# Kernel optimization log

Measured on AMD Instinct MI355X. Metric: run time of the kernel, lower is better.

The kernel has to match this reference:

```python
import jax, jax.numpy as jnp
import numpy as np

N, D, E, H, TOP_K = 4096, 1024, 8, 2048, 2


def setup_inputs() -> dict:
    key = jax.random.key(0)
    kx, kr, k1, kb1, k2, kb2 = jax.random.split(key, 6)
    x = jax.random.normal(kx, (N, D), dtype=jnp.float32)
    # top-2 sparse routing scores: zeros mark non-routed (token, expert) pairs
    r = jax.random.uniform(kr, (N, E), dtype=jnp.float32)
    thresh = jax.lax.top_k(r, TOP_K)[0][:, -1:]
    routing = jnp.where(r >= thresh, r, 0.0)
    # Expert params, torch Linear init scale (uniform +-1/sqrt(fan_in))
    s1 = 1.0 / np.sqrt(D)
    s2 = 1.0 / np.sqrt(H)
    W1 = jax.random.uniform(k1, (E, D, H), dtype=jnp.float32, minval=-s1, maxval=s1)
    b1 = jax.random.uniform(kb1, (E, H), dtype=jnp.float32, minval=-s1, maxval=s1)
    W2 = jax.random.uniform(k2, (E, H, D), dtype=jnp.float32, minval=-s2, maxval=s2)
    b2 = jax.random.uniform(kb2, (E, D), dtype=jnp.float32, minval=-s2, maxval=s2)
    return {"x": x, "routing": routing, "W1": W1, "b1": b1, "W2": W2, "b2": b2}


def reference(x, routing, W1, b1, W2, b2):
    # Each expert is Linear(D,H) -> GELU -> Linear(H,D); per-token output is
    # sum over experts of routing[n,e] * expert_e(x[n]). Tokens with routing==0
    # contribute exactly zero, matching the masked gather/scatter in the original.
    h = jax.nn.gelu(jnp.einsum('nd,edh->neh', x, W1) + b1[None], approximate=False)  # [N,E,H]
    y = jnp.einsum('neh,ehd->ned', h, W2) + b2[None]                                  # [N,E,D]
    return jnp.einsum('ned,ne->nd', y, routing)                                       # [N,D]
```

## Files before the change

kernel.cpp:

```cpp
#include <hip/hip_runtime.h>
#include <hip/hip_bf16.h>

#define NTOK 4096
#define DIM  1024
#define NEXP 8
#define HID  2048
#define HROWS 8448

typedef __attribute__((ext_vector_type(8))) __bf16 bf16x8;
typedef __attribute__((ext_vector_type(4))) float  f32x4;
typedef __attribute__((address_space(1))) const unsigned char gconst_u8;
typedef __attribute__((address_space(3))) unsigned char lds_u8;

__device__ __forceinline__ unsigned short f2bf(float f) {
    unsigned u = __float_as_uint(f);
    u += 0x7fffu + ((u >> 16) & 1u);
    return (unsigned short)(u >> 16);
}

__device__ __forceinline__ void gload16(const void* g, void* l) {
    __builtin_amdgcn_global_load_lds((gconst_u8*)g, (lds_u8*)l, 16, 0, 0);
}

#define WAITK(N) asm volatile("s_waitcnt vmcnt(" #N ") lgkmcnt(0)" ::: "memory")
#define BAR() do { __builtin_amdgcn_s_barrier(); __builtin_amdgcn_sched_barrier(0); } while (0)

__global__ __launch_bounds__(256) void prep(
    const float* __restrict__ x, const float* __restrict__ routing,
    const float* __restrict__ W1,
    unsigned short* __restrict__ xbf, unsigned short* __restrict__ W1F,
    int* __restrict__ counts, int* __restrict__ lists,
    int* __restrict__ slotrec, int* __restrict__ scnt)
{
    const int bid = blockIdx.x;
    const int t = threadIdx.x;
    if (bid >= 4096) {
        int n = (bid - 4096) * 256 + t;
        if (n >= NTOK) return;
        int sc = 0;
        #pragma unroll
        for (int e = 0; e < NEXP; ++e) {
            if (routing[n * NEXP + e] > 0.0f) {
                int i = atomicAdd(&counts[e], 1);
                if (i < NTOK) {
                    lists[e * NTOK + i] = n;
                    if (sc < 4) slotrec[n * 4 + sc] = (e << 20) | i;
                    ++sc;
                }
            }
        }
        scnt[n] = sc;
        return;
    }
    if (bid >= 2048) {
        int i = ((bid - 2048) * 256 + t) * 8;
        float4 a = *(const float4*)(x + i);
        float4 b = *(const float4*)(x + i + 4);
        unsigned short v[8];
        v[0] = f2bf(a.x); v[1] = f2bf(a.y); v[2] = f2bf(a.z); v[3] = f2bf(a.w);
        v[4] = f2bf(b.x); v[5] = f2bf(b.y); v[6] = f2bf(b.z); v[7] = f2bf(b.w);
        *(uint4*)(xbf + i) = *(const uint4*)v;
        return;
    }
    int e = bid >> 8, ks = (bid >> 3) & 31, fblk = bid & 7;
    const float* src = W1 + ((size_t)e * DIM + ks * 32) * HID + fblk * 256;
    unsigned short* dst = W1F + (((size_t)(e * 32 + ks) * 128) + fblk * 16) * 512;
    __shared__ unsigned short lds[32][264];
    const int kr = t >> 3, ch = t & 7;
    #pragma unroll
    for (int q = 0; q < 8; ++q) {
        float4 f4 = *(const float4*)(src + (size_t)kr * HID + ch * 32 + q * 4);
        int c = ch * 32 + q * 4;
        lds[kr][c + 0] = f2bf(f4.x); lds[kr][c + 1] = f2bf(f4.y);
        lds[kr][c + 2] = f2bf(f4.z); lds[kr][c + 3] = f2bf(f4.w);
    }
    __syncthreads();
    uint4* dv = (uint4*)dst;
    #pragma unroll
    for (int i = 0; i < 4; ++i) {
        int Q = t + 256 * i;
        int fl = Q >> 6, l = Q & 63;
        int cb = fl * 16 + (l & 15), rb = (l >> 4) * 8;
        unsigned short v[8];
        #pragma unroll
        for (int j = 0; j < 8; ++j) v[j] = lds[rb + j][cb];
        dv[Q] = *(const uint4*)v;
    }
}

__global__ __launch_bounds__(512, 4) void gemm1_gelu(
    const unsigned short* __restrict__ xbf, const unsigned short* __restrict__ W1F,
    const float* __restrict__ b1, const int* __restrict__ counts,
    const int* __restrict__ lists, unsigned short* __restrict__ h,
    const float* __restrict__ W2, unsigned short* __restrict__ W2F)
{
    __shared__ uint4 SM[4608];
    const int bid = blockIdx.x;
    const int t = threadIdx.x;

    if (bid >= 768) {
        const int unit = bid - 768;
        const int e = unit & 7, ks = (unit >> 3) & 63, half = unit >> 9;
        const float* src = W2 + ((size_t)e * HID + ks * 32) * DIM + half * 512;
        unsigned short* lds = (unsigned short*)SM;
        const int kr = t >> 4, ch = t & 15;
        #pragma unroll
        for (int q = 0; q < 8; ++q) {
            float4 f4 = *(const float4*)(src + (size_t)kr * DIM + ch * 32 + q * 4);
            int c = ch * 32 + q * 4;
            lds[kr * 520 + c + 0] = f2bf(f4.x); lds[kr * 520 + c + 1] = f2bf(f4.y);
            lds[kr * 520 + c + 2] = f2bf(f4.z); lds[kr * 520 + c + 3] = f2bf(f4.w);
        }
        __syncthreads();
        uint4* dv = (uint4*)(W2F + (((size_t)(e * 64 + ks)) * 64 + half * 32) * 512);
        #pragma unroll
        for (int i = 0; i < 4; ++i) {
            int Q = t + 512 * i;
            int fl = Q >> 6, l = Q & 63;
            int cb = fl * 16 + (l & 15), rb = (l >> 4) * 8;
            unsigned short v[8];
            #pragma unroll
            for (int j = 0; j < 8; ++j) v[j] = lds[(rb + j) * 520 + cb];
            dv[Q] = *(const uint4*)v;
        }
        return;
    }

    const int e  = bid & 7;
    const int q  = bid >> 3;
    const int mt = q % 6;
    const int nt = q / 6;

    int cnt = counts[e];
    int off = 0;
    #pragma unroll
    for (int j = 0; j < NEXP; ++j) if (j < e) off += counts[j];
    if (off + cnt > HROWS) cnt = HROWS - off;
    const int m0 = mt * 256;
    if (m0 >= cnt) return;

    const int lane = t & 63;
    const int wid  = t >> 6;
    const int wm   = wid >> 1;
    const int wn   = wid & 1;

    const int gi0 = m0 + wid * 16 + (lane & 15);
    const int gi1 = gi0 + 128;
    const int tok0 = lists[e * NTOK + ((gi0 < cnt) ? gi0 : 0)];
    const int tok1 = lists[e * NTOK + ((gi1 < cnt) ? gi1 : 0)];
    const unsigned short* ag0 = xbf + (size_t)tok0 * DIM + (lane >> 4) * 8;
    const unsigned short* ag1 = xbf + (size_t)tok1 * DIM + (lane >> 4) * 8;

    const unsigned short* bg = W1F + ((size_t)(e * 32) * 128 + nt * 8 + wid) * 512 + lane * 8;

    f32x4 acc[4][4];
    #pragma unroll
    for (int m = 0; m < 4; ++m)
        #pragma unroll
        for (int n = 0; n < 4; ++n) acc[m][n] = (f32x4){0.f, 0.f, 0.f, 0.f};

#define STG1(P, KS) do { \
        gload16(ag0 + (KS) * 32, (P) + wid * 64); \
        gload16(ag1 + (KS) * 32, (P) + (wid + 8) * 64); \
        gload16(bg + (size_t)(KS) * 65536, (P) + 1024 + wid * 64); \
    } while (0)
#define CMP1(P) do { \
        const bf16x8* Af = (const bf16x8*)(P); \
        const bf16x8* Bf = (const bf16x8*)((P) + 1024); \
        bf16x8 af[4], bfr[4]; \
        _Pragma("unroll") for (int m = 0; m < 4; ++m) af[m] = Af[((wm * 4 + m) << 6) | lane]; \
        _Pragma("unroll") for (int n = 0; n < 4; ++n) bfr[n] = Bf[((wn * 4 + n) << 6) | lane]; \
        __builtin_amdgcn_s_setprio(1); \
        _Pragma("unroll") for (int m = 0; m < 4; ++m) \
            _Pragma("unroll") for (int n = 0; n < 4; ++n) \
                acc[m][n] = __builtin_amdgcn_mfma_f32_16x16x32_bf16(af[m], bfr[n], acc[m][n], 0, 0, 0); \
        __builtin_amdgcn_s_setprio(0); \
    } while (0)

    uint4 *P0 = SM, *P1 = SM + 1536, *P2 = SM + 3072;
    STG1(P0, 0);
    STG1(P1, 1);
    for (int T = 0; T < 30; ++T) {
        WAITK(3);
        BAR();
        STG1(P2, T + 2);
        CMP1(P0);
        uint4* tmp = P0; P0 = P1; P1 = P2; P2 = tmp;
    }
    WAITK(3); BAR(); CMP1(P0);
    { uint4* tmp = P0; P0 = P1; P1 = P2; P2 = tmp; }
    WAITK(0); BAR(); CMP1(P0);
#undef STG1
#undef CMP1

    asm volatile("s_waitcnt lgkmcnt(0)" ::: "memory");
    BAR();
    unsigned short* hb = (unsigned short*)SM;
    const int lg = lane >> 4;
    #pragma unroll
    for (int n = 0; n < 4; ++n) {
        const int cl = (wn * 4 + n) * 16 + (lane & 15);
        const float bb = b1[e * HID + nt * 128 + cl];
        #pragma unroll
        for (int m = 0; m < 4; ++m) {
            const int il = (wm * 4 + m) * 16 + (lg << 2);
            const int scl = cl ^ (lg << 4);
            #pragma unroll
            for (int r = 0; r < 4; ++r) {
                float v = acc[m][n][r] + bb;
                float g = 0.5f * v * (1.0f + erff(v * 0.70710678118654752f));
                hb[(il + r) * 144 + scl] = f2bf(g);
            }
        }
    }
    __syncthreads();
    #pragma unroll
    for (int s = 0; s < 8; ++s) {
        const int row = s * 32 + (t >> 4);
        if (m0 + row < cnt) {
            const int p = t & 15;
            const int gblk = ((p >> 1) ^ ((row >> 2) & 3));
            const int gc = gblk * 16 + (p & 1) * 8;
            uint4 v = *(const uint4*)(hb + row * 144 + p * 8);
            *(uint4*)(h + (size_t)(off + m0 + row) * HID + nt * 128 + gc) = v;
        }
    }
}

__global__ __launch_bounds__(256, 4) void gemm2_store(
    const unsigned short* __restrict__ h, const unsigned short* __restrict__ W2F,
    const float* __restrict__ b2, const int* __restrict__ counts,
    const int* __restrict__ lists, const float* __restrict__ routing,
    float* __restrict__ cbuf)
{
    const int id = blockIdx.x;
    const int e  = id & 7;
    const int nt = (id >> 3) & 7;
    const int mt = id >> 6;

    int cnt = counts[e];
    int off = 0;
    #pragma unroll
    for (int j = 0; j < NEXP; ++j) if (j < e) off += counts[j];
    if (off + cnt > HROWS) cnt = HROWS - off;
    const int m0 = mt * 128;
    if (m0 >= cnt) return;

    __shared__ uint4 SM[3072];

    const int t    = threadIdx.x;
    const int lane = t & 63;
    const int wid  = t >> 6;
    const int wm   = wid >> 1;
    const int wn   = wid & 1;

    const int r0 = off + m0 + wid * 16 + (lane & 15);
    const unsigned short* ag0 = h + (size_t)r0 * HID + (lane >> 4) * 8;
    const unsigned short* ag1 = ag0 + (size_t)64 * HID;

    const unsigned short* bg0 = W2F + ((size_t)(e * 64) * 64 + nt * 8 + wid) * 512 + lane * 8;
    const unsigned short* bg1 = bg0 + 4 * 512;

    f32x4 acc[4][4];
    #pragma unroll
    for (int m = 0; m < 4; ++m)
        #pragma unroll
        for (int n = 0; n < 4; ++n) acc[m][n] = (f32x4){0.f, 0.f, 0.f, 0.f};

#define STG2(P, KS) do { \
        gload16(ag0 + (KS) * 32, (P) + wid * 64); \
        gload16(ag1 + (KS) * 32, (P) + (wid + 4) * 64); \
        gload16(bg0 + (size_t)(KS) * 32768, (P) + 512 + wid * 64); \
        gload16(bg1 + (size_t)(KS) * 32768, (P) + 512 + (wid + 4) * 64); \
    } while (0)
#define CMP2(P) do { \
        const bf16x8* Af = (const bf16x8*)(P); \
        const bf16x8* Bf = (const bf16x8*)((P) + 512); \
        bf16x8 af[4], bfr[4]; \
        _Pragma("unroll") for (int m = 0; m < 4; ++m) af[m] = Af[((wm * 4 + m) << 6) | lane]; \
        _Pragma("unroll") for (int n = 0; n < 4; ++n) bfr[n] = Bf[((wn * 4 + n) << 6) | lane]; \
        __builtin_amdgcn_s_setprio(1); \
        _Pragma("unroll") for (int m = 0; m < 4; ++m) \
            _Pragma("unroll") for (int n = 0; n < 4; ++n) \
                acc[m][n] = __builtin_amdgcn_mfma_f32_16x16x32_bf16(af[m], bfr[n], acc[m][n], 0, 0, 0); \
        __builtin_amdgcn_s_setprio(0); \
    } while (0)

    uint4 *P0 = SM, *P1 = SM + 1024, *P2 = SM + 2048;
    STG2(P0, 0);
    STG2(P1, 1);
    for (int T = 0; T < 62; ++T) {
        WAITK(4);
        BAR();
        STG2(P2, T + 2);
        CMP2(P0);
        uint4* tmp = P0; P0 = P1; P1 = P2; P2 = tmp;
    }
    WAITK(4); BAR(); CMP2(P0);
    { uint4* tmp = P0; P0 = P1; P1 = P2; P2 = tmp; }
    WAITK(0); BAR(); CMP2(P0);
#undef STG2
#undef CMP2

    const int n0 = nt * 128;
    int cols[4]; float bb[4];
    #pragma unroll
    for (int n = 0; n < 4; ++n) {
        cols[n] = n0 + (wn * 4 + n) * 16 + (lane & 15);
        bb[n] = b2[e * DIM + cols[n]];
    }
    #pragma unroll
    for (int m = 0; m < 4; ++m) {
        const int ib = m0 + (wm * 4 + m) * 16 + ((lane >> 4) << 2);
        #pragma unroll
        for (int r = 0; r < 4; ++r) {
            const int i = ib + r;
            if (i < cnt) {
                const int token = lists[e * NTOK + i];
                const float wt = routing[token * NEXP + e];
                float* dst = cbuf + (size_t)(off + i) * DIM;
                #pragma unroll
                for (int n = 0; n < 4; ++n)
                    dst[cols[n]] = wt * (acc[m][n][r] + bb[n]);
            }
        }
    }
}

__global__ __launch_bounds__(256) void combine(
    const float* __restrict__ cbuf, const int* __restrict__ counts,
    const int* __restrict__ slotrec, const int* __restrict__ scnt,
    float* __restrict__ out)
{
    const int n = blockIdx.x;
    const int t = threadIdx.x;
    int offs[NEXP];
    int s = 0;
    #pragma unroll
    for (int e = 0; e < NEXP; ++e) { offs[e] = s; s += counts[e]; }
    int sc = scnt[n]; if (sc > 4) sc = 4;
    float4 acc = {0.f, 0.f, 0.f, 0.f};
    for (int j = 0; j < sc; ++j) {
        int rec = slotrec[n * 4 + j];
        int e = rec >> 20, i = rec & 0xFFFFF;
        float4 v = ((const float4*)(cbuf + (size_t)(offs[e] + i) * DIM))[t];
        acc.x += v.x; acc.y += v.y; acc.z += v.z; acc.w += v.w;
    }
    ((float4*)(out + (size_t)n * DIM))[t] = acc;
}

extern "C" void kernel_launch(void* const* d_in, const int* in_sizes, int n_in,
                              void* d_out, int out_size, void* d_ws, size_t ws_size,
                              hipStream_t stream) {
    const float* x       = (const float*)d_in[0];
    const float* routing = (const float*)d_in[1];
    const float* W1      = (const float*)d_in[2];
    const float* b1      = (const float*)d_in[3];
    const float* W2      = (const float*)d_in[4];
    const float* b2      = (const float*)d_in[5];
    float* out = (float*)d_out;

    char* ws = (char*)d_ws;
    int* counts          = (int*)ws;
    int* lists           = (int*)(ws + 0x400);
    int* slotrec         = (int*)(ws + 0x20400);
    int* scnt            = (int*)(ws + 0x30400);
    unsigned short* xbf  = (unsigned short*)(ws + 0x40000);
    float*          cbuf = (float*)(ws + 0x40000);
    unsigned short* W1F  = (unsigned short*)(ws + 0x840000);
    unsigned short* W2F  = (unsigned short*)(ws + 0x2840000);
    unsigned short* h    = (unsigned short*)(ws + 0x4840000);

    hipMemsetAsync(counts, 0, 256, stream);
    prep<<<4112, 256, 0, stream>>>(x, routing, W1, xbf, W1F,
                                   counts, lists, slotrec, scnt);
    gemm1_gelu<<<1792, 512, 0, stream>>>(xbf, W1F, b1, counts, lists, h, W2, W2F);
    gemm2_store<<<768, 256, 0, stream>>>(h, W2F, b2, counts, lists, routing, cbuf);
    combine<<<NTOK, 256, 0, stream>>>(cbuf, counts, slotrec, scnt, out);
}
```

Before: 185.4 us.

## Load A operand directly into registers, stage only B through LDS

In both expert GEMM kernels the A operand (gathered token rows of xbf, or rows of h) is no longer staged through LDS. Each wave loads its own fragments straight into registers with vector global loads, and only the B weight tiles keep the triple-buffered global_load_lds pipeline. The A loads are issued after each compute step, and the wait counts are adjusted to match. This cuts LDS traffic and footprint, which could raise occupancy, but the A loads are now duplicated across the wn waves and have less latency hiding. The prep kernels also pad their LDS transpose rows differently to avoid bank conflicts.

New measurement: 281.3 us. +51.7%, slower.

```diff
diff --git a/kernel.cpp b/kernel.cpp
--- a/kernel.cpp
+++ b/kernel.cpp
@@ -24,6 +24,7 @@
 
 #define WAITK(N) asm volatile("s_waitcnt vmcnt(" #N ") lgkmcnt(0)" ::: "memory")
 #define BAR() do { __builtin_amdgcn_s_barrier(); __builtin_amdgcn_sched_barrier(0); } while (0)
+#define SFENCE() __builtin_amdgcn_sched_barrier(0)
 
 __global__ __launch_bounds__(256) void prep(
     const float* __restrict__ x, const float* __restrict__ routing,
@@ -65,7 +66,7 @@
     int e = bid >> 8, ks = (bid >> 3) & 31, fblk = bid & 7;
     const float* src = W1 + ((size_t)e * DIM + ks * 32) * HID + fblk * 256;
     unsigned short* dst = W1F + (((size_t)(e * 32 + ks) * 128) + fblk * 16) * 512;
-    __shared__ unsigned short lds[32][264];
+    __shared__ unsigned short lds[32][266];
     const int kr = t >> 3, ch = t & 7;
     #pragma unroll
     for (int q = 0; q < 8; ++q) {
@@ -108,8 +109,8 @@
         for (int q = 0; q < 8; ++q) {
             float4 f4 = *(const float4*)(src + (size_t)kr * DIM + ch * 32 + q * 4);
             int c = ch * 32 + q * 4;
-            lds[kr * 520 + c + 0] = f2bf(f4.x); lds[kr * 520 + c + 1] = f2bf(f4.y);
-            lds[kr * 520 + c + 2] = f2bf(f4.z); lds[kr * 520 + c + 3] = f2bf(f4.w);
+            lds[kr * 522 + c + 0] = f2bf(f4.x); lds[kr * 522 + c + 1] = f2bf(f4.y);
+            lds[kr * 522 + c + 2] = f2bf(f4.z); lds[kr * 522 + c + 3] = f2bf(f4.w);
         }
         __syncthreads();
         uint4* dv = (uint4*)(W2F + (((size_t)(e * 64 + ks)) * 64 + half * 32) * 512);
@@ -120,7 +121,7 @@
             int cb = fl * 16 + (l & 15), rb = (l >> 4) * 8;
             unsigned short v[8];
             #pragma unroll
-            for (int j = 0; j < 8; ++j) v[j] = lds[(rb + j) * 520 + cb];
+            for (int j = 0; j < 8; ++j) v[j] = lds[(rb + j) * 522 + cb];
             dv[Q] = *(const uint4*)v;
         }
         return;
@@ -143,13 +144,15 @@
     const int wid  = t >> 6;
     const int wm   = wid >> 1;
     const int wn   = wid & 1;
-
-    const int gi0 = m0 + wid * 16 + (lane & 15);
-    const int gi1 = gi0 + 128;
-    const int tok0 = lists[e * NTOK + ((gi0 < cnt) ? gi0 : 0)];
-    const int tok1 = lists[e * NTOK + ((gi1 < cnt) ? gi1 : 0)];
-    const unsigned short* ag0 = xbf + (size_t)tok0 * DIM + (lane >> 4) * 8;
-    const unsigned short* ag1 = xbf + (size_t)tok1 * DIM + (lane >> 4) * 8;
+    const int lane15 = lane & 15;
+
+    unsigned aoff[4];
+    #pragma unroll
+    for (int m = 0; m < 4; ++m) {
+        int r = m0 + (wm * 4 + m) * 16 + lane15;
+        int tok = lists[e * NTOK + ((r < cnt) ? r : 0)];
+        aoff[m] = (unsigned)tok * DIM + ((lane >> 4) << 3);
+    }
 
     const unsigned short* bg = W1F + ((size_t)(e * 32) * 128 + nt * 8 + wid) * 512 + lane * 8;
 
@@ -159,37 +162,43 @@
         #pragma unroll
         for (int n = 0; n < 4; ++n) acc[m][n] = (f32x4){0.f, 0.f, 0.f, 0.f};
 
-#define STG1(P, KS) do { \
-        gload16(ag0 + (KS) * 32, (P) + wid * 64); \
-        gload16(ag1 + (KS) * 32, (P) + (wid + 8) * 64); \
-        gload16(bg + (size_t)(KS) * 65536, (P) + 1024 + wid * 64); \
+    bf16x8 ar[4];
+
+#define LDA1(KS) do { \
+        _Pragma("unroll") for (int m = 0; m < 4; ++m) \
+            ar[m] = *(const bf16x8*)(xbf + aoff[m] + (KS) * 32); \
     } while (0)
+#define STG1(P, KS) gload16(bg + (size_t)(KS) * 65536, (P) + wid * 64)
 #define CMP1(P) do { \
-        const bf16x8* Af = (const bf16x8*)(P); \
-        const bf16x8* Bf = (const bf16x8*)((P) + 1024); \
-        bf16x8 af[4], bfr[4]; \
-        _Pragma("unroll") for (int m = 0; m < 4; ++m) af[m] = Af[((wm * 4 + m) << 6) | lane]; \
+        const bf16x8* Bf = (const bf16x8*)(P); \
+        bf16x8 bfr[4]; \
         _Pragma("unroll") for (int n = 0; n < 4; ++n) bfr[n] = Bf[((wn * 4 + n) << 6) | lane]; \
         __builtin_amdgcn_s_setprio(1); \
         _Pragma("unroll") for (int m = 0; m < 4; ++m) \
             _Pragma("unroll") for (int n = 0; n < 4; ++n) \
-                acc[m][n] = __builtin_amdgcn_mfma_f32_16x16x32_bf16(af[m], bfr[n], acc[m][n], 0, 0, 0); \
+                acc[m][n] = __builtin_amdgcn_mfma_f32_16x16x32_bf16(ar[m], bfr[n], acc[m][n], 0, 0, 0); \
         __builtin_amdgcn_s_setprio(0); \
     } while (0)
 
-    uint4 *P0 = SM, *P1 = SM + 1536, *P2 = SM + 3072;
-    STG1(P0, 0);
+    uint4 *P0 = SM, *P1 = SM + 512, *P2 = SM + 1024;
+    STG1(P0, 0); SFENCE();
+    LDA1(0);     SFENCE();
     STG1(P1, 1);
     for (int T = 0; T < 30; ++T) {
-        WAITK(3);
+        WAITK(1);
         BAR();
+        CMP1(P0); SFENCE();
+        LDA1(T + 1); SFENCE();
         STG1(P2, T + 2);
-        CMP1(P0);
         uint4* tmp = P0; P0 = P1; P1 = P2; P2 = tmp;
     }
-    WAITK(3); BAR(); CMP1(P0);
+    WAITK(1); BAR();
+    CMP1(P0); SFENCE();
+    LDA1(31);
     { uint4* tmp = P0; P0 = P1; P1 = P2; P2 = tmp; }
-    WAITK(0); BAR(); CMP1(P0);
+    WAITK(0); BAR();
+    CMP1(P0);
+#undef LDA1
 #undef STG1
 #undef CMP1
 
@@ -246,17 +255,21 @@
     const int m0 = mt * 128;
     if (m0 >= cnt) return;
 
-    __shared__ uint4 SM[3072];
+    __shared__ uint4 SM[1536];
 
     const int t    = threadIdx.x;
     const int lane = t & 63;
     const int wid  = t >> 6;
     const int wm   = wid >> 1;
     const int wn   = wid & 1;
-
-    const int r0 = off + m0 + wid * 16 + (lane & 15);
-    const unsigned short* ag0 = h + (size_t)r0 * HID + (lane >> 4) * 8;
-    const unsigned short* ag1 = ag0 + (size_t)64 * HID;
+    const int lane15 = lane & 15;
+
+    unsigned aoff[4];
+    #pragma unroll
+    for (int m = 0; m < 4; ++m) {
+        int rr = off + m0 + (wm * 4 + m) * 16 + lane15;
+        aoff[m] = (unsigned)rr * HID + ((lane >> 4) << 3);
+    }
 
     const unsigned short* bg0 = W2F + ((size_t)(e * 64) * 64 + nt * 8 + wid) * 512 + lane * 8;
     const unsigned short* bg1 = bg0 + 4 * 512;
@@ -267,38 +280,46 @@
         #pragma unroll
         for (int n = 0; n < 4; ++n) acc[m][n] = (f32x4){0.f, 0.f, 0.f, 0.f};
 
+    bf16x8 ar[4];
+
+#define LDA2(KS) do { \
+        _Pragma("unroll") for (int m = 0; m < 4; ++m) \
+            ar[m] = *(const bf16x8*)(h + aoff[m] + (KS) * 32); \
+    } while (0)
 #define STG2(P, KS) do { \
-        gload16(ag0 + (KS) * 32, (P) + wid * 64); \
-        gload16(ag1 + (KS) * 32, (P) + (wid + 4) * 64); \
-        gload16(bg0 + (size_t)(KS) * 32768, (P) + 512 + wid * 64); \
-        gload16(bg1 + (size_t)(KS) * 32768, (P) + 512 + (wid + 4) * 64); \
+        gload16(bg0 + (size_t)(KS) * 32768, (P) + wid * 64); \
+        gload16(bg1 + (size_t)(KS) * 32768, (P) + (wid + 4) * 64); \
     } while (0)
 #define CMP2(P) do { \
-        const bf16x8* Af = (const bf16x8*)(P); \
-        const bf16x8* Bf = (const bf16x8*)((P) + 512); \
-        bf16x8 af[4], bfr[4]; \
-        _Pragma("unroll") for (int m = 0; m < 4; ++m) af[m] = Af[((wm * 4 + m) << 6) | lane]; \
+        const bf16x8* Bf = (const bf16x8*)(P); \
+        bf16x8 bfr[4]; \
         _Pragma("unroll") for (int n = 0; n < 4; ++n) bfr[n] = Bf[((wn * 4 + n) << 6) | lane]; \
         __builtin_amdgcn_s_setprio(1); \
         _Pragma("unroll") for (int m = 0; m < 4; ++m) \
             _Pragma("unroll") for (int n = 0; n < 4; ++n) \
-                acc[m][n] = __builtin_amdgcn_mfma_f32_16x16x32_bf16(af[m], bfr[n], acc[m][n], 0, 0, 0); \
+                acc[m][n] = __builtin_amdgcn_mfma_f32_16x16x32_bf16(ar[m], bfr[n], acc[m][n], 0, 0, 0); \
         __builtin_amdgcn_s_setprio(0); \
     } while (0)
 
-    uint4 *P0 = SM, *P1 = SM + 1024, *P2 = SM + 2048;
-    STG2(P0, 0);
+    uint4 *P0 = SM, *P1 = SM + 512, *P2 = SM + 1024;
+    STG2(P0, 0); SFENCE();
+    LDA2(0);     SFENCE();
     STG2(P1, 1);
     for (int T = 0; T < 62; ++T) {
-        WAITK(4);
+        WAITK(2);
         BAR();
+        CMP2(P0); SFENCE();
+        LDA2(T + 1); SFENCE();
         STG2(P2, T + 2);
-        CMP2(P0);
         uint4* tmp = P0; P0 = P1; P1 = P2; P2 = tmp;
     }
-    WAITK(4); BAR(); CMP2(P0);
+    WAITK(2); BAR();
+    CMP2(P0); SFENCE();
+    LDA2(63);
     { uint4* tmp = P0; P0 = P1; P1 = P2; P2 = tmp; }
-    WAITK(0); BAR(); CMP2(P0);
+    WAITK(0); BAR();
+    CMP2(P0);
+#undef LDA2
 #undef STG2
 #undef CMP2
 
```

## Fuse combine into gemm2 via atomicAdd scatter and pad LDS transpose rows

Applied to the files above, without the earlier changes.

Drops the separate combine kernel and the intermediate cbuf: gemm2 now atomically adds each routed row's weighted expert output straight into the zero-initialised output, indexed by token. This saves one launch plus writing and re-reading an 8448x1024 fp32 buffer, at the cost of a memset of the output and scalar fp32 atomics, which contend when both experts for a token land on the same address. Separately, the LDS row pitch of the W1/W2 bf16 transpose staging goes from 264/520 to 266/522 elements to reduce bank conflicts on the column-wise reads. Atomic summation order makes the result non-deterministic in the last bits.

Measured after the change: 189.5 us. 1.02x slower.

```diff
diff --git a/kernel.cpp b/kernel.cpp
--- a/kernel.cpp
+++ b/kernel.cpp
@@ -65,7 +65,7 @@
     int e = bid >> 8, ks = (bid >> 3) & 31, fblk = bid & 7;
     const float* src = W1 + ((size_t)e * DIM + ks * 32) * HID + fblk * 256;
     unsigned short* dst = W1F + (((size_t)(e * 32 + ks) * 128) + fblk * 16) * 512;
-    __shared__ unsigned short lds[32][264];
+    __shared__ unsigned short lds[32][266];
     const int kr = t >> 3, ch = t & 7;
     #pragma unroll
     for (int q = 0; q < 8; ++q) {
@@ -108,8 +108,8 @@
         for (int q = 0; q < 8; ++q) {
             float4 f4 = *(const float4*)(src + (size_t)kr * DIM + ch * 32 + q * 4);
             int c = ch * 32 + q * 4;
-            lds[kr * 520 + c + 0] = f2bf(f4.x); lds[kr * 520 + c + 1] = f2bf(f4.y);
-            lds[kr * 520 + c + 2] = f2bf(f4.z); lds[kr * 520 + c + 3] = f2bf(f4.w);
+            lds[kr * 522 + c + 0] = f2bf(f4.x); lds[kr * 522 + c + 1] = f2bf(f4.y);
+            lds[kr * 522 + c + 2] = f2bf(f4.z); lds[kr * 522 + c + 3] = f2bf(f4.w);
         }
         __syncthreads();
         uint4* dv = (uint4*)(W2F + (((size_t)(e * 64 + ks)) * 64 + half * 32) * 512);
@@ -120,7 +120,7 @@
             int cb = fl * 16 + (l & 15), rb = (l >> 4) * 8;
             unsigned short v[8];
             #pragma unroll
-            for (int j = 0; j < 8; ++j) v[j] = lds[(rb + j) * 520 + cb];
+            for (int j = 0; j < 8; ++j) v[j] = lds[(rb + j) * 522 + cb];
             dv[Q] = *(const uint4*)v;
         }
         return;
@@ -231,7 +231,7 @@
     const unsigned short* __restrict__ h, const unsigned short* __restrict__ W2F,
     const float* __restrict__ b2, const int* __restrict__ counts,
     const int* __restrict__ lists, const float* __restrict__ routing,
-    float* __restrict__ cbuf)
+    float* __restrict__ out)
 {
     const int id = blockIdx.x;
     const int e  = id & 7;
@@ -318,35 +318,13 @@
             if (i < cnt) {
                 const int token = lists[e * NTOK + i];
                 const float wt = routing[token * NEXP + e];
-                float* dst = cbuf + (size_t)(off + i) * DIM;
+                float* dst = out + (size_t)token * DIM;
                 #pragma unroll
                 for (int n = 0; n < 4; ++n)
-                    dst[cols[n]] = wt * (acc[m][n][r] + bb[n]);
+                    atomicAdd(&dst[cols[n]], wt * (acc[m][n][r] + bb[n]));
             }
         }
     }
-}
-
-__global__ __launch_bounds__(256) void combine(
-    const float* __restrict__ cbuf, const int* __restrict__ counts,
-    const int* __restrict__ slotrec, const int* __restrict__ scnt,
-    float* __restrict__ out)
-{
-    const int n = blockIdx.x;
-    const int t = threadIdx.x;
-    int offs[NEXP];
-    int s = 0;
-    #pragma unroll
-    for (int e = 0; e < NEXP; ++e) { offs[e] = s; s += counts[e]; }
-    int sc = scnt[n]; if (sc > 4) sc = 4;
-    float4 acc = {0.f, 0.f, 0.f, 0.f};
-    for (int j = 0; j < sc; ++j) {
-        int rec = slotrec[n * 4 + j];
-        int e = rec >> 20, i = rec & 0xFFFFF;
-        float4 v = ((const float4*)(cbuf + (size_t)(offs[e] + i) * DIM))[t];
-        acc.x += v.x; acc.y += v.y; acc.z += v.z; acc.w += v.w;
-    }
-    ((float4*)(out + (size_t)n * DIM))[t] = acc;
 }
 
 extern "C" void kernel_launch(void* const* d_in, const int* in_sizes, int n_in,
@@ -366,15 +344,14 @@
     int* slotrec         = (int*)(ws + 0x20400);
     int* scnt            = (int*)(ws + 0x30400);
     unsigned short* xbf  = (unsigned short*)(ws + 0x40000);
-    float*          cbuf = (float*)(ws + 0x40000);
     unsigned short* W1F  = (unsigned short*)(ws + 0x840000);
     unsigned short* W2F  = (unsigned short*)(ws + 0x2840000);
     unsigned short* h    = (unsigned short*)(ws + 0x4840000);
 
     hipMemsetAsync(counts, 0, 256, stream);
+    hipMemsetAsync(out, 0, (size_t)NTOK * DIM * sizeof(float), stream);
     prep<<<4112, 256, 0, stream>>>(x, routing, W1, xbf, W1F,
                                    counts, lists, slotrec, scnt);
     gemm1_gelu<<<1792, 512, 0, stream>>>(xbf, W1F, b1, counts, lists, h, W2, W2F);
-    gemm2_store<<<768, 256, 0, stream>>>(h, W2F, b2, counts, lists, routing, cbuf);
-    combine<<<NTOK, 256, 0, stream>>>(cbuf, counts, slotrec, scnt, out);
-}
+    gemm2_store<<<768, 256, 0, stream>>>(h, W2F, b2, counts, lists, routing, out);
+}
```

## Switch GEMM pipelines from triple to double buffering to cut LDS footprint

Applied to the files above, without the earlier changes.

Both GEMM kernels move from a three-stage LDS ring with a prefetch distance of two to a two-buffer ping-pong with a prefetch distance of one. This shrinks shared memory per block, which can raise occupancy. The gemm1 epilogue writes the 256-row GELU tile in two 128-row passes so it fits the smaller buffer. Transpose padding in the weight-conversion paths also changes from 264/520 to 266/522 to alter LDS bank mapping. The cost is less latency hiding, since each iteration now waits for all outstanding loads, plus extra barriers in the epilogue.

Measured after the change: 203.6 us. +9.8%, slower.

```diff
diff --git a/kernel.cpp b/kernel.cpp
--- a/kernel.cpp
+++ b/kernel.cpp
@@ -65,7 +65,7 @@
     int e = bid >> 8, ks = (bid >> 3) & 31, fblk = bid & 7;
     const float* src = W1 + ((size_t)e * DIM + ks * 32) * HID + fblk * 256;
     unsigned short* dst = W1F + (((size_t)(e * 32 + ks) * 128) + fblk * 16) * 512;
-    __shared__ unsigned short lds[32][264];
+    __shared__ unsigned short lds[32][266];
     const int kr = t >> 3, ch = t & 7;
     #pragma unroll
     for (int q = 0; q < 8; ++q) {
@@ -94,7 +94,7 @@
     const int* __restrict__ lists, unsigned short* __restrict__ h,
     const float* __restrict__ W2, unsigned short* __restrict__ W2F)
 {
-    __shared__ uint4 SM[4608];
+    __shared__ uint4 SM[3072];
     const int bid = blockIdx.x;
     const int t = threadIdx.x;
 
@@ -108,8 +108,8 @@
         for (int q = 0; q < 8; ++q) {
             float4 f4 = *(const float4*)(src + (size_t)kr * DIM + ch * 32 + q * 4);
             int c = ch * 32 + q * 4;
-            lds[kr * 520 + c + 0] = f2bf(f4.x); lds[kr * 520 + c + 1] = f2bf(f4.y);
-            lds[kr * 520 + c + 2] = f2bf(f4.z); lds[kr * 520 + c + 3] = f2bf(f4.w);
+            lds[kr * 522 + c + 0] = f2bf(f4.x); lds[kr * 522 + c + 1] = f2bf(f4.y);
+            lds[kr * 522 + c + 2] = f2bf(f4.z); lds[kr * 522 + c + 3] = f2bf(f4.w);
         }
         __syncthreads();
         uint4* dv = (uint4*)(W2F + (((size_t)(e * 64 + ks)) * 64 + half * 32) * 512);
@@ -120,7 +120,7 @@
             int cb = fl * 16 + (l & 15), rb = (l >> 4) * 8;
             unsigned short v[8];
             #pragma unroll
-            for (int j = 0; j < 8; ++j) v[j] = lds[(rb + j) * 520 + cb];
+            for (int j = 0; j < 8; ++j) v[j] = lds[(rb + j) * 522 + cb];
             dv[Q] = *(const uint4*)v;
         }
         return;
@@ -177,19 +177,17 @@
         __builtin_amdgcn_s_setprio(0); \
     } while (0)
 
-    uint4 *P0 = SM, *P1 = SM + 1536, *P2 = SM + 3072;
-    STG1(P0, 0);
-    STG1(P1, 1);
-    for (int T = 0; T < 30; ++T) {
-        WAITK(3);
+    uint4 *Pc = SM, *Pn = SM + 1536;
+    STG1(Pc, 0);
+    WAITK(0); BAR();
+    for (int T = 0; T < 31; ++T) {
+        STG1(Pn, T + 1);
+        CMP1(Pc);
+        WAITK(0);
         BAR();
-        STG1(P2, T + 2);
-        CMP1(P0);
-        uint4* tmp = P0; P0 = P1; P1 = P2; P2 = tmp;
-    }
-    WAITK(3); BAR(); CMP1(P0);
-    { uint4* tmp = P0; P0 = P1; P1 = P2; P2 = tmp; }
-    WAITK(0); BAR(); CMP1(P0);
+        uint4* tmp = Pc; Pc = Pn; Pn = tmp;
+    }
+    CMP1(Pc);
 #undef STG1
 #undef CMP1
 
@@ -198,32 +196,39 @@
     unsigned short* hb = (unsigned short*)SM;
     const int lg = lane >> 4;
     #pragma unroll
-    for (int n = 0; n < 4; ++n) {
-        const int cl = (wn * 4 + n) * 16 + (lane & 15);
-        const float bb = b1[e * HID + nt * 128 + cl];
-        #pragma unroll
-        for (int m = 0; m < 4; ++m) {
-            const int il = (wm * 4 + m) * 16 + (lg << 2);
-            const int scl = cl ^ (lg << 4);
+    for (int pass = 0; pass < 2; ++pass) {
+        if ((wm >> 1) == pass) {
             #pragma unroll
-            for (int r = 0; r < 4; ++r) {
-                float v = acc[m][n][r] + bb;
-                float g = 0.5f * v * (1.0f + erff(v * 0.70710678118654752f));
-                hb[(il + r) * 144 + scl] = f2bf(g);
+            for (int n = 0; n < 4; ++n) {
+                const int cl = (wn * 4 + n) * 16 + (lane & 15);
+                const float bb = b1[e * HID + nt * 128 + cl];
+                #pragma unroll
+                for (int m = 0; m < 4; ++m) {
+                    const int il = (wm & 1) * 64 + m * 16 + (lg << 2);
+                    const int scl = cl ^ (lg << 4);
+                    #pragma unroll
+                    for (int r = 0; r < 4; ++r) {
+                        float v = acc[m][n][r] + bb;
+                        float g = 0.5f * v * (1.0f + erff(v * 0.70710678118654752f));
+                        hb[(il + r) * 144 + scl] = f2bf(g);
+                    }
+                }
             }
         }
-    }
-    __syncthreads();
-    #pragma unroll
-    for (int s = 0; s < 8; ++s) {
-        const int row = s * 32 + (t >> 4);
-        if (m0 + row < cnt) {
-            const int p = t & 15;
-            const int gblk = ((p >> 1) ^ ((row >> 2) & 3));
-            const int gc = gblk * 16 + (p & 1) * 8;
-            uint4 v = *(const uint4*)(hb + row * 144 + p * 8);
-            *(uint4*)(h + (size_t)(off + m0 + row) * HID + nt * 128 + gc) = v;
-        }
+        __syncthreads();
+        #pragma unroll
+        for (int s = 0; s < 4; ++s) {
+            const int row = s * 32 + (t >> 4);
+            const int grow = m0 + pass * 128 + row;
+            if (grow < cnt) {
+                const int p = t & 15;
+                const int gblk = ((p >> 1) ^ ((row >> 2) & 3));
+                const int gc = gblk * 16 + (p & 1) * 8;
+                uint4 v = *(const uint4*)(hb + row * 144 + p * 8);
+                *(uint4*)(h + (size_t)(off + grow) * HID + nt * 128 + gc) = v;
+            }
+        }
+        __syncthreads();
     }
 }
 
@@ -246,7 +251,7 @@
     const int m0 = mt * 128;
     if (m0 >= cnt) return;
 
-    __shared__ uint4 SM[3072];
+    __shared__ uint4 SM[2048];
 
     const int t    = threadIdx.x;
     const int lane = t & 63;
@@ -286,19 +291,17 @@
         __builtin_amdgcn_s_setprio(0); \
     } while (0)
 
-    uint4 *P0 = SM, *P1 = SM + 1024, *P2 = SM + 2048;
-    STG2(P0, 0);
-    STG2(P1, 1);
-    for (int T = 0; T < 62; ++T) {
-        WAITK(4);
+    uint4 *Pc = SM, *Pn = SM + 1024;
+    STG2(Pc, 0);
+    WAITK(0); BAR();
+    for (int T = 0; T < 63; ++T) {
+        STG2(Pn, T + 1);
+        CMP2(Pc);
+        WAITK(0);
         BAR();
-        STG2(P2, T + 2);
-        CMP2(P0);
-        uint4* tmp = P0; P0 = P1; P1 = P2; P2 = tmp;
-    }
-    WAITK(4); BAR(); CMP2(P0);
-    { uint4* tmp = P0; P0 = P1; P1 = P2; P2 = tmp; }
-    WAITK(0); BAR(); CMP2(P0);
+        uint4* tmp = Pc; Pc = Pn; Pn = tmp;
+    }
+    CMP2(Pc);
 #undef STG2
 #undef CMP2
 
```
